# Optimization experiments

Measured on AMD Instinct MI355X. Metric: run time of the kernel, lower is better.

The kernel has to match this reference:

```python
import jax, jax.numpy as jnp
import numpy as np

B = 4
D = H = W = 128
N = 500_000
CIN = 32
COUT = 32
K = 5
EPS = 1e-4


def setup_inputs() -> dict:
    # unique voxel coordinates (submanifold sparse tensor sites)
    rng = np.random.default_rng(0)
    flat = rng.choice(B * D * H * W, size=N, replace=False)
    b = flat // (D * H * W)
    rem = flat % (D * H * W)
    z = rem // (H * W)
    rem2 = rem % (H * W)
    y = rem2 // W
    x = rem2 % W
    coords = jnp.asarray(np.stack([b, z, y, x], axis=1).astype(np.int32))  # [N,4]

    key = jax.random.key(0)
    k1, k2, k3, k4 = jax.random.split(key, 4)
    features = jax.random.normal(k1, (N, CIN), jnp.float32)
    gamma = 1.0 + 0.1 * jax.random.normal(k2, (CIN,), jnp.float32)
    beta = 0.1 * jax.random.normal(k3, (CIN,), jnp.float32)
    weight = jax.random.normal(k4, (K ** 3, CIN, COUT), jnp.float32) / np.sqrt(K ** 3 * CIN)
    return {"features": features, "coords": coords, "gamma": gamma, "beta": beta, "weight": weight}


def _subm_conv(feats, coords, weight):
    # dense site-index grid: flat voxel id -> row in feats (-1 if inactive)
    flat_idx = ((coords[:, 0] * D + coords[:, 1]) * H + coords[:, 2]) * W + coords[:, 3]
    grid = jnp.full((B * D * H * W,), -1, jnp.int32).at[flat_idx].set(
        jnp.arange(N, dtype=jnp.int32))

    r = jnp.arange(-(K // 2), K // 2 + 1, dtype=jnp.int32)
    offs = jnp.stack(jnp.meshgrid(r, r, r, indexing="ij"), axis=-1).reshape(-1, 3)  # [125,3] (dz,dy,dx)
    bounds = jnp.array([D, H, W], jnp.int32)

    def body(acc, off_w):
        off, w = off_w
        nb = coords[:, 1:] + off  # [N,3]
        inb = jnp.all((nb >= 0) & (nb < bounds), axis=1)
        nflat = ((coords[:, 0] * D + nb[:, 0]) * H + nb[:, 1]) * W + nb[:, 2]
        nidx = jnp.where(inb, grid[jnp.clip(nflat, 0, B * D * H * W - 1)], -1)
        valid = nidx >= 0
        g = jnp.where(valid[:, None], feats[jnp.clip(nidx, 0, N - 1)], 0.0)  # [N,CIN]
        return acc + g @ w, None

    acc, _ = jax.lax.scan(body, jnp.zeros((N, COUT), feats.dtype), (offs, weight))
    return acc


def reference(features, coords, gamma, beta, weight):
    # BatchNorm1d over active sites (training-mode batch stats, biased var)
    mean = jnp.mean(features, axis=0)
    var = jnp.mean(jnp.square(features - mean), axis=0)
    xhat = (features - mean) * jax.lax.rsqrt(var + EPS)
    y = jax.nn.relu(xhat * gamma + beta)
    # submanifold sparse 3D conv, kernel 5, padding 2, no bias
    return _subm_conv(y, coords, weight)
```

## Files before the change

### kernel.cpp

```cpp
#include <hip/hip_runtime.h>

typedef unsigned short u16;
typedef unsigned int u32;
typedef unsigned long long u64;

#define N_SITES 500000
#define CIN 32
#define COUT 32
#define DD 128
#define HHH 128
#define WWW 128
#define KVOL 125
#define EPSV 1e-4f
#define NVOX (4*DD*HHH*WWW)
#define RED_BLOCKS 504
#define CNT_BLOCKS 8192
#define NSLOT 500224
#define ZROW  N_SITES
#define SENTI (NVOX+4)

typedef short v8s __attribute__((ext_vector_type(8)));
typedef float v16f __attribute__((ext_vector_type(16)));

__device__ __forceinline__ u16 f2bf(float f){
  union { float f; u32 i; } v; v.f = f;
  u32 r = v.i + 0x7fffu + ((v.i >> 16) & 1u);
  return (u16)(r >> 16);
}

__launch_bounds__(256)
__global__ void bn_reduce(const float* __restrict__ x, float* __restrict__ partial){
  __shared__ float ssum[8][32], ssq[8][32];
  int tid = threadIdx.x;
  int c   = tid & 31;
  int row = tid >> 5;
  float s = 0.f, q = 0.f;
  for(int site = blockIdx.x*8 + row; site < N_SITES; site += gridDim.x*8){
    float f = x[(size_t)site*32 + c];
    s += f; q += f*f;
  }
  ssum[row][c] = s; ssq[row][c] = q;
  __syncthreads();
  if(tid < 32){
    float ts = 0.f, tq = 0.f;
    #pragma unroll
    for(int r = 0; r < 8; r++){ ts += ssum[r][tid]; tq += ssq[r][tid]; }
    partial[blockIdx.x*64 + tid]      = ts;
    partial[blockIdx.x*64 + 32 + tid] = tq;
  }
}

__global__ void bn_finalize_pad(const float* __restrict__ partial, const float* __restrict__ gamma,
                                const float* __restrict__ beta, float* __restrict__ ss, int nblk,
                                int* __restrict__ perm, u32* __restrict__ yzero){
  int tid = threadIdx.x;
  if(tid < 32){
    float s = 0.f, q = 0.f;
    for(int b = 0; b < nblk; b++){
      s += partial[b*64 + tid];
      q += partial[b*64 + 32 + tid];
    }
    float mean = s / (float)N_SITES;
    float var  = q / (float)N_SITES - mean*mean;
    float scale = gamma[tid] * rsqrtf(var + EPSV);
    ss[tid]      = scale;
    ss[32 + tid] = beta[tid] - mean*scale;
  }
  if(tid < NSLOT - N_SITES) perm[N_SITES + tid] = perm[0];
  if(tid < 16) yzero[tid] = 0;
}

__launch_bounds__(256)
__global__ void bn_apply_y(const float4* __restrict__ xv, const float* __restrict__ ss,
                           const int* __restrict__ rank, uint4* __restrict__ yv){
  __shared__ float sc[64];
  int tid = threadIdx.x;
  if(tid < 64) sc[tid] = ss[tid];
  __syncthreads();
  const int total = N_SITES*CIN/8;
  int stride = gridDim.x*256;
  for(int i = blockIdx.x*256 + tid; i < total; i += stride){
    int c0 = (i & 3) * 8;
    int slot = rank[i >> 2];
    float4 a = xv[2*i], b = xv[2*i+1];
    float f[8] = {a.x,a.y,a.z,a.w,b.x,b.y,b.z,b.w};
    #pragma unroll
    for(int j = 0; j < 8; j++) f[j] = fmaxf(f[j]*sc[c0+j] + sc[32+c0+j], 0.f);
    uint4 o;
    o.x = ((u32)f2bf(f[1])<<16) | f2bf(f[0]);
    o.y = ((u32)f2bf(f[3])<<16) | f2bf(f[2]);
    o.z = ((u32)f2bf(f[5])<<16) | f2bf(f[4]);
    o.w = ((u32)f2bf(f[7])<<16) | f2bf(f[6]);
    yv[slot*4 + (i & 3)] = o;
  }
}

__launch_bounds__(256)
__global__ void build_grid(const int4* __restrict__ coords, int* __restrict__ grid){
  int i = blockIdx.x*256 + threadIdx.x;
  if(i >= N_SITES) return;
  int4 c = coords[i];
  grid[((c.x*DD + c.y)*HHH + c.z)*WWW + c.w] = i;
}

__launch_bounds__(256)
__global__ void count_blocks(const int* __restrict__ grid, int* __restrict__ blockcnt){
  int b = blockIdx.x, t = threadIdx.x;
  int cnt = 0;
  #pragma unroll
  for(int k = 0; k < 4; k++) cnt += (grid[b*1024 + k*256 + t] >= 0);
  #pragma unroll
  for(int o = 32; o > 0; o >>= 1) cnt += __shfl_down(cnt, o);
  __shared__ int wsum[4];
  if((t & 63) == 0) wsum[t >> 6] = cnt;
  __syncthreads();
  if(t == 0) blockcnt[b] = wsum[0] + wsum[1] + wsum[2] + wsum[3];
}

__launch_bounds__(1024)
__global__ void scan_blocks(const int* __restrict__ blockcnt, int* __restrict__ blockoff){
  __shared__ int s[1024];
  int t = threadIdx.x;
  int loc[8]; int v = 0;
  #pragma unroll
  for(int k = 0; k < 8; k++){ loc[k] = blockcnt[t*8 + k]; v += loc[k]; }
  s[t] = v; __syncthreads();
  for(int o = 1; o < 1024; o <<= 1){
    int add = (t >= o) ? s[t - o] : 0;
    __syncthreads();
    s[t] += add;
    __syncthreads();
  }
  int base = s[t] - v;
  #pragma unroll
  for(int k = 0; k < 8; k++){ blockoff[t*8 + k] = base; base += loc[k]; }
}

__launch_bounds__(256)
__global__ void fill_perm(int* __restrict__ grid, const int* __restrict__ blockoff,
                          int* __restrict__ perm, int* __restrict__ rank){
  int b = blockIdx.x, t = threadIdx.x;
  int w = t >> 6, lane = t & 63;
  __shared__ int wcnt[4];
  __shared__ int carry;
  if(t == 0) carry = 0;
  __syncthreads();
  int base = blockoff[b];
  for(int p = 0; p < 4; p++){
    int v = b*1024 + p*256 + t;
    int s = grid[v];
    bool act = (s >= 0);
    u64 bal = __ballot(act);
    int pre = (int)__popcll(bal & ((1ull << lane) - 1ull));
    if(lane == 0) wcnt[w] = (int)__popcll(bal);
    __syncthreads();
    int woff = 0;
    for(int ww = 0; ww < w; ww++) woff += wcnt[ww];
    if(act){
      int slot = base + carry + woff + pre;
      perm[slot] = s;
      rank[s] = slot;
      grid[v] = slot;
    }
    int tot = wcnt[0] + wcnt[1] + wcnt[2] + wcnt[3];
    __syncthreads();
    if(t == 0) carry += tot;
    __syncthreads();
  }
}

__launch_bounds__(256)
__global__ void prep_wfrag(const float* __restrict__ w, u16* __restrict__ wf){
  int i = blockIdx.x*256 + threadIdx.x;
  if(i >= KVOL*2*64*8) return;
  int j    = i & 7;
  int lane = (i >> 3) & 63;
  int half = (i >> 9) & 1;
  int off  = i >> 10;
  int k = half*16 + ((lane >> 5) << 3) + j;
  int n = lane & 31;
  wf[i] = f2bf(w[off*1024 + k*32 + n]);
}

__launch_bounds__(256)
__global__ void conv_mfma(const u16* __restrict__ y, const int4* __restrict__ coords,
                          const u16* __restrict__ wf, const int* __restrict__ gridp,
                          const int* __restrict__ perm, float* __restrict__ out){
  const char* __restrict__ yc  = (const char*)y;
  const char* __restrict__ gcp = (const char*)gridp;
  __shared__ v8s swf[3200];

  int t = threadIdx.x;
  int l = t & 63;
  int r31 = l & 31;
  int h = l >> 5;
  u32 koff = (u32)h << 4;

  int nwg = gridDim.x, bid = blockIdx.x;
  int xcd = bid & 7, rk = bid >> 3;
  int q8 = nwg >> 3, r8 = nwg & 7;
  int swz = (xcd < r8 ? xcd*(q8+1) : r8*(q8+1) + (xcd - r8)*q8) + rk;

  int slot = swz*256 + t;
  int p = perm[slot];
  int4 c = coords[p];
  int Z = c.y, Y = c.z, X = c.w;
  int base = ((c.x*DD + Z)*HHH + Y)*WWW + X;

  int b0 = __shfl(base, r31);
  int b1 = __shfl(base, 32 + r31);
  int x0 = __shfl(X, r31),  x1 = __shfl(X, 32 + r31);
  int y0 = __shfl(Y, r31),  y1 = __shfl(Y, 32 + r31);
  int z0 = __shfl(Z, r31),  z1 = __shfl(Z, 32 + r31);

  bool okx0[5], okx1[5], oky0[5], oky1[5];
  #pragma unroll
  for(int k = 0; k < 5; k++){
    okx0[k] = (u32)(x0 + k - 2) < WWW;
    okx1[k] = (u32)(x1 + k - 2) < WWW;
    oky0[k] = (u32)(y0 + k - 2) < HHH;
    oky1[k] = (u32)(y1 + k - 2) < HHH;
  }

  v16f acc0, acc1;
  #pragma unroll
  for(int i = 0; i < 16; i++){ acc0[i] = 0.f; acc1[i] = 0.f; }

  const int HW = HHH*WWW;
  const uint4* __restrict__ wfv = (const uint4*)wf;

#define PROBE_WIN(rr) { \
    bool zy0 = okz0 && oky0[rr]; \
    bool zy1 = okz1 && oky1[rr]; \
    int st0 = zy0 ? (pb0 + ((rr)-2)*WWW - 2) : SENTI; \
    int st1 = zy1 ? (pb1 + ((rr)-2)*WWW - 2) : SENTI; \
    int al0 = st0 & ~3, al1 = st1 & ~3; \
    sh0 = st0 - al0; sh1 = st1 - al1; \
    rA0 = *(const int4*)(gcp + (long)al0*4); \
    rA1 = *(const int4*)(gcp + (long)al0*4 + 16); \
    rB0 = *(const int4*)(gcp + (long)al1*4); \
    rB1 = *(const int4*)(gcp + (long)al1*4 + 16); \
  }

#define EXTRACT(rr) { \
    int e0[8] = {rA0.x,rA0.y,rA0.z,rA0.w,rA1.x,rA1.y,rA1.z,rA1.w}; \
    int e1[8] = {rB0.x,rB0.y,rB0.z,rB0.w,rB1.x,rB1.y,rB1.z,rB1.w}; \
    bool sa2 = (sh0 & 2) != 0, sa1 = (sh0 & 1) != 0; \
    bool sb2 = (sh1 & 2) != 0, sb1 = (sh1 & 1) != 0; \
    _Pragma("unroll") \
    for(int k = 0; k < 5; k++){ \
      int t0 = sa2 ? e0[k+2] : e0[k]; \
      int t1 = sa2 ? e0[k+3] : e0[k+1]; \
      nvA[k] = okx0[k] ? (sa1 ? t1 : t0) : -1; \
      int u0 = sb2 ? e1[k+2] : e1[k]; \
      int u1 = sb2 ? e1[k+3] : e1[k+1]; \
      nvB[k] = okx1[k] ? (sb1 ? u1 : u0) : -1; \
    } \
  }

  #pragma unroll 1
  for(int dz = -2; dz <= 2; dz++){
    bool okz0 = (u32)(z0 + dz) < DD;
    bool okz1 = (u32)(z1 + dz) < DD;
    int pb0 = b0 + dz*HW, pb1 = b1 + dz*HW;

    int4 rA0, rA1, rB0, rB1;
    int sh0, sh1;
    PROBE_WIN(0)
    asm volatile("" ::: "memory");

    __syncthreads();
    {
      u32 pbase = (u32)((dz + 2) * 3200);
      #pragma unroll
      for(int it = 0; it < 13; it++){
        int ch = it*256 + t;
        if(ch < 3200){
          uint4 v = wfv[pbase + ch];
          *(uint4*)&swf[ch] = v;
        }
      }
    }
    __syncthreads();

    #pragma unroll
    for(int r = 0; r < 5; r++){
      int nvA[5], nvB[5];
      EXTRACT(r)
      v8s fr[20];
      #pragma unroll
      for(int k = 0; k < 5; k++){
        u32 n0 = (u32)nvA[k], n1 = (u32)nvB[k];
        u32 rw0 = n0 < (u32)ZROW ? n0 : (u32)ZROW;
        u32 rw1 = n1 < (u32)ZROW ? n1 : (u32)ZROW;
        u32 ya0 = (rw0 << 6) + koff;
        u32 ya1 = (rw1 << 6) + koff;
        fr[k*4+0] = *(const v8s*)(yc + ya0);
        fr[k*4+1] = *(const v8s*)(yc + ya0 + 32u);
        fr[k*4+2] = *(const v8s*)(yc + ya1);
        fr[k*4+3] = *(const v8s*)(yc + ya1 + 32u);
      }
      asm volatile("" ::: "memory");
      if(r < 4){
        PROBE_WIN(r+1)
        asm volatile("" ::: "memory");
      }
      #pragma unroll
      for(int k = 0; k < 5; k++){
        int o = r*5 + k;
        v8s wb0 = swf[o*128 + l];
        v8s wb1 = swf[o*128 + 64 + l];
        acc0 = __builtin_amdgcn_mfma_f32_32x32x16_bf16(fr[k*4+0], wb0, acc0, 0, 0, 0);
        acc0 = __builtin_amdgcn_mfma_f32_32x32x16_bf16(fr[k*4+1], wb1, acc0, 0, 0, 0);
        acc1 = __builtin_amdgcn_mfma_f32_32x32x16_bf16(fr[k*4+2], wb0, acc1, 0, 0, 0);
        acc1 = __builtin_amdgcn_mfma_f32_32x32x16_bf16(fr[k*4+3], wb1, acc1, 0, 0, 0);
      }
    }
  }
#undef PROBE_WIN
#undef EXTRACT

  #pragma unroll
  for(int rg = 0; rg < 16; rg++){
    int row = (rg & 3) + ((rg >> 2) << 3) + (h << 2);
    int s0 = __shfl(p, row);
    int s1 = __shfl(p, 32 + row);
    out[(size_t)s0*32 + r31] = acc0[rg];
    out[(size_t)s1*32 + r31] = acc1[rg];
  }
}

extern "C" void kernel_launch(void* const* d_in, const int* in_sizes, int n_in,
                              void* d_out, int out_size, void* d_ws, size_t ws_size,
                              hipStream_t stream) {
  const float* feats  = (const float*)d_in[0];
  const int4*  coords = (const int4*) d_in[1];
  const float* gamma  = (const float*)d_in[2];
  const float* beta   = (const float*)d_in[3];
  const float* wght   = (const float*)d_in[4];
  float* out = (float*)d_out;

  char* ws = (char*)d_ws;
  int*   grid_raw = (int*)  ws;
  int*   gridp    = grid_raw + 8;
  u16*   yperm    = (u16*)  (ws + 33554560);
  u16*   wf       = (u16*)  (ws + 65554624);
  int*   perm     = (int*)  (ws + 65810624);
  int*   blockcnt = (int*)  (ws + 67811520);
  int*   blockoff = (int*)  (ws + 67844288);
  float* partial  = (float*)(ws + 67877056);
  float* ss       = (float*)(ws + 68006080);
  int* rank = (int*)d_out;

  hipMemsetAsync(grid_raw, 0xFF, (size_t)(NVOX+32)*4, stream);

  build_grid  <<<(N_SITES+255)/256, 256, 0, stream>>>(coords, gridp);
  count_blocks<<<CNT_BLOCKS, 256, 0, stream>>>(gridp, blockcnt);
  scan_blocks <<<1, 1024, 0, stream>>>(blockcnt, blockoff);
  fill_perm   <<<CNT_BLOCKS, 256, 0, stream>>>(gridp, blockoff, perm, rank);

  bn_reduce      <<<RED_BLOCKS, 256, 0, stream>>>(feats, partial);
  bn_finalize_pad<<<1, 256, 0, stream>>>(partial, gamma, beta, ss, RED_BLOCKS,
                                         perm, (u32*)(yperm + (size_t)ZROW*32));
  bn_apply_y <<<2048, 256, 0, stream>>>((const float4*)feats, ss, rank, (uint4*)yperm);

  prep_wfrag<<<(KVOL*2*64*8 + 255)/256, 256, 0, stream>>>(wght, wf);

  conv_mfma<<<NSLOT/256, 256, 0, stream>>>(yperm, coords, wf, gridp, perm, out);
}
```

Before: 537.2 us.

## Read conv weights directly from global, drop LDS staging and barriers; parallelize reductions

The conv kernel no longer stages each dz-slice of bf16 weight fragments into shared memory behind two block barriers. Each wave now loads its weight fragments straight from global memory (cached in L1/L2) per row, and launch bounds request 4 waves per SIMD. This removes the LDS staging and syncs in exchange for more global or cache traffic and register pressure. The BN finalize reduction is spread over 256 threads, and the block scan switches to wave-level shuffles instead of a barrier-heavy Hillis-Steele scan.

```diff
diff --git a/kernel.cpp b/kernel.cpp
--- a/kernel.cpp
+++ b/kernel.cpp
@@ -53,15 +53,22 @@
 __global__ void bn_finalize_pad(const float* __restrict__ partial, const float* __restrict__ gamma,
                                 const float* __restrict__ beta, float* __restrict__ ss, int nblk,
                                 int* __restrict__ perm, u32* __restrict__ yzero){
+  __shared__ float red[8][64];
   int tid = threadIdx.x;
+  int c = tid & 31, r = tid >> 5;
+  float s = 0.f, q = 0.f;
+  for(int b = r; b < nblk; b += 8){
+    s += partial[b*64 + c];
+    q += partial[b*64 + 32 + c];
+  }
+  red[r][c] = s; red[r][32 + c] = q;
+  __syncthreads();
   if(tid < 32){
-    float s = 0.f, q = 0.f;
-    for(int b = 0; b < nblk; b++){
-      s += partial[b*64 + tid];
-      q += partial[b*64 + 32 + tid];
-    }
-    float mean = s / (float)N_SITES;
-    float var  = q / (float)N_SITES - mean*mean;
+    float ts = 0.f, tq = 0.f;
+    #pragma unroll
+    for(int rr = 0; rr < 8; rr++){ ts += red[rr][tid]; tq += red[rr][32 + tid]; }
+    float mean = ts / (float)N_SITES;
+    float var  = tq / (float)N_SITES - mean*mean;
     float scale = gamma[tid] * rsqrtf(var + EPSV);
     ss[tid]      = scale;
     ss[32 + tid] = beta[tid] - mean*scale;
@@ -119,19 +126,31 @@
 
 __launch_bounds__(1024)
 __global__ void scan_blocks(const int* __restrict__ blockcnt, int* __restrict__ blockoff){
-  __shared__ int s[1024];
+  __shared__ int wsum[16];
   int t = threadIdx.x;
+  int lane = t & 63, w = t >> 6;
   int loc[8]; int v = 0;
   #pragma unroll
   for(int k = 0; k < 8; k++){ loc[k] = blockcnt[t*8 + k]; v += loc[k]; }
-  s[t] = v; __syncthreads();
-  for(int o = 1; o < 1024; o <<= 1){
-    int add = (t >= o) ? s[t - o] : 0;
-    __syncthreads();
-    s[t] += add;
-    __syncthreads();
-  }
-  int base = s[t] - v;
+  int s = v;
+  #pragma unroll
+  for(int o = 1; o < 64; o <<= 1){
+    int u = __shfl_up(s, o);
+    if(lane >= o) s += u;
+  }
+  if(lane == 63) wsum[w] = s;
+  __syncthreads();
+  if(w == 0 && lane < 16){
+    int x = wsum[lane];
+    #pragma unroll
+    for(int o = 1; o < 16; o <<= 1){
+      int u = __shfl_up(x, o);
+      if(lane >= o) x += u;
+    }
+    wsum[lane] = x;
+  }
+  __syncthreads();
+  int base = s - v + (w > 0 ? wsum[w - 1] : 0);
   #pragma unroll
   for(int k = 0; k < 8; k++){ blockoff[t*8 + k] = base; base += loc[k]; }
 }
@@ -182,13 +201,13 @@
   wf[i] = f2bf(w[off*1024 + k*32 + n]);
 }
 
-__launch_bounds__(256)
+__launch_bounds__(256, 4)
 __global__ void conv_mfma(const u16* __restrict__ y, const int4* __restrict__ coords,
                           const u16* __restrict__ wf, const int* __restrict__ gridp,
                           const int* __restrict__ perm, float* __restrict__ out){
   const char* __restrict__ yc  = (const char*)y;
   const char* __restrict__ gcp = (const char*)gridp;
-  __shared__ v8s swf[3200];
+  const v8s*  __restrict__ wfv8 = (const v8s*)wf;
 
   int t = threadIdx.x;
   int l = t & 63;
@@ -227,7 +246,6 @@
   for(int i = 0; i < 16; i++){ acc0[i] = 0.f; acc1[i] = 0.f; }
 
   const int HW = HHH*WWW;
-  const uint4* __restrict__ wfv = (const uint4*)wf;
 
 #define PROBE_WIN(rr) { \
     bool zy0 = okz0 && oky0[rr]; \
@@ -269,22 +287,15 @@
     PROBE_WIN(0)
     asm volatile("" ::: "memory");
 
-    __syncthreads();
-    {
-      u32 pbase = (u32)((dz + 2) * 3200);
+    #pragma unroll
+    for(int r = 0; r < 5; r++){
+      const v8s* wrow = wfv8 + (u32)(((dz + 2)*5 + r)*5) * 128u;
+      v8s wb[10];
       #pragma unroll
-      for(int it = 0; it < 13; it++){
-        int ch = it*256 + t;
-        if(ch < 3200){
-          uint4 v = wfv[pbase + ch];
-          *(uint4*)&swf[ch] = v;
-        }
+      for(int k = 0; k < 5; k++){
+        wb[k*2+0] = wrow[k*128 + l];
+        wb[k*2+1] = wrow[k*128 + 64 + l];
       }
-    }
-    __syncthreads();
-
-    #pragma unroll
-    for(int r = 0; r < 5; r++){
       int nvA[5], nvB[5];
       EXTRACT(r)
       v8s fr[20];
@@ -307,13 +318,10 @@
       }
       #pragma unroll
       for(int k = 0; k < 5; k++){
-        int o = r*5 + k;
-        v8s wb0 = swf[o*128 + l];
-        v8s wb1 = swf[o*128 + 64 + l];
-        acc0 = __builtin_amdgcn_mfma_f32_32x32x16_bf16(fr[k*4+0], wb0, acc0, 0, 0, 0);
-        acc0 = __builtin_amdgcn_mfma_f32_32x32x16_bf16(fr[k*4+1], wb1, acc0, 0, 0, 0);
-        acc1 = __builtin_amdgcn_mfma_f32_32x32x16_bf16(fr[k*4+2], wb0, acc1, 0, 0, 0);
-        acc1 = __builtin_amdgcn_mfma_f32_32x32x16_bf16(fr[k*4+3], wb1, acc1, 0, 0, 0);
+        acc0 = __builtin_amdgcn_mfma_f32_32x32x16_bf16(fr[k*4+0], wb[k*2+0], acc0, 0, 0, 0);
+        acc0 = __builtin_amdgcn_mfma_f32_32x32x16_bf16(fr[k*4+1], wb[k*2+1], acc0, 0, 0, 0);
+        acc1 = __builtin_amdgcn_mfma_f32_32x32x16_bf16(fr[k*4+2], wb[k*2+0], acc1, 0, 0, 0);
+        acc1 = __builtin_amdgcn_mfma_f32_32x32x16_bf16(fr[k*4+3], wb[k*2+1], acc1, 0, 0, 0);
       }
     }
   }
```

Result: faster. 464.0 us (-13.6%).
